# Kernel tuning notes

Measured on AMD Instinct MI355X. Metric: run time of the kernel, lower is better.

The kernel has to match this reference:

```python
import jax, jax.numpy as jnp
import numpy as np

B, T, D, NH = 4, 2048, 1024, 16
HD = D // NH


def setup_inputs() -> dict:
    key = jax.random.key(0)
    ks = jax.random.split(key, 6)
    scale = 0.02
    x = jax.random.normal(ks[0], (B, T, D), dtype=jnp.float32)
    Wr = jax.random.normal(ks[1], (D, D), dtype=jnp.float32) * scale
    Wk = jax.random.normal(ks[2], (D, D), dtype=jnp.float32) * scale
    Wv = jax.random.normal(ks[3], (D, D), dtype=jnp.float32) * scale
    Ww = jax.random.normal(ks[4], (D, D), dtype=jnp.float32) * scale
    Wo = jax.random.normal(ks[5], (D, D), dtype=jnp.float32) * scale
    return {"x": x, "Wr": Wr, "Wk": Wk, "Wv": Wv, "Ww": Ww, "Wo": Wo}


def _rwkv7_forward(x, Wr, Wk, Wv, Ww, Wo):
    b, t, d = x.shape
    nh, hd = NH, d // NH
    # projections (F.linear: x @ W.T), no bias
    r = jax.nn.sigmoid(x @ Wr.T).reshape(b, t, nh, hd)
    k = (x @ Wk.T).reshape(b, t, nh, hd)
    v = (x @ Wv.T).reshape(b, t, nh, hd)
    w = (jax.nn.sigmoid(x @ Ww.T) * 0.99).reshape(b, t, nh, hd)

    def step(state, inp):
        # state: [B, nh, hd_v, hd_k]
        w_t, k_t, v_t, r_t = inp  # each [B, nh, hd]
        state = state * w_t[..., :, None] + v_t[..., :, None] * k_t[..., None, :]
        out_t = r_t * state.sum(-1)  # [B, nh, hd]
        return state, out_t

    seq = (jnp.moveaxis(w, 1, 0), jnp.moveaxis(k, 1, 0),
           jnp.moveaxis(v, 1, 0), jnp.moveaxis(r, 1, 0))  # time-major
    state0 = jnp.zeros((b, nh, hd, hd), dtype=x.dtype)
    _, outs = jax.lax.scan(step, state0, seq)  # [T, B, nh, hd]
    out = jnp.moveaxis(outs, 0, 1).reshape(b, t, d)

    # RMSNorm with eps=None -> torch uses dtype eps
    eps = jnp.asarray(jnp.finfo(out.dtype).eps, out.dtype)
    out = out * jax.lax.rsqrt(jnp.mean(out * out, axis=-1, keepdims=True) + eps)
    return out @ Wo.T


def reference(x, Wr, Wk, Wv, Ww, Wo):
    return _rwkv7_forward(x, Wr, Wk, Wv, Ww, Wo)
```

## Files before the change

### kernel.cpp

```cpp
#include <hip/hip_runtime.h>
#include <hip/hip_bf16.h>
#include <stdint.h>


#define BB 4
#define TT 2048
#define DD 1024
#define NHH 16
#define HDD 64
#define CC 64
#define LL 32
#define NCH 4096

using bf16 = __hip_bfloat16;
typedef __attribute__((ext_vector_type(8))) short bfrag8;
typedef __attribute__((ext_vector_type(4))) float f32x4;

__device__ __forceinline__ void async_ld16(const bf16* g, bf16* l) {
  __builtin_amdgcn_global_load_lds(
      (const __attribute__((address_space(1))) uint32_t*)g,
      (__attribute__((address_space(3))) uint32_t*)l, 16, 0, 0);
}

__device__ __forceinline__ float sigm(float x) {
  return __builtin_amdgcn_rcpf(1.0f + __expf(-x));
}
__device__ __forceinline__ float bf2f(bf16 h) {
  unsigned short u = *reinterpret_cast<unsigned short*>(&h);
  return __uint_as_float((unsigned)u << 16);
}
__device__ __forceinline__ unsigned short f2bfbits(float f) {
  bf16 b = __float2bfloat16(f);
  return *reinterpret_cast<unsigned short*>(&b);
}

__global__ __launch_bounds__(256)
void convert_kernel(const float* __restrict__ x,
                    const float* __restrict__ Wr, const float* __restrict__ Wv,
                    const float* __restrict__ Ww, const float* __restrict__ Wo,
                    const float* __restrict__ Wk,
                    bf16* __restrict__ x_c, bf16* __restrict__ W_c,
                    float* __restrict__ wks)
{
  if (blockIdx.x >= 12288) {
    const int gid = (blockIdx.x - 12288) * 256 + threadIdx.x;
    const int h = gid >> 10, c = gid & 1023;
    float s = 0.0f;
    for (int j = 0; j < 64; ++j)
      s += Wk[(long)((h << 6) + j) * 1024 + c];
    wks[gid] = s;
    return;
  }
  const long g = (long)blockIdx.x * 256 + threadIdx.x;
  const float* src; bf16* dst; long off4;
  if (g < 2097152) { src = x; dst = x_c; off4 = g; }
  else {
    long gg = g - 2097152;
    int wsel = (int)(gg >> 18);
    off4 = gg & 262143;
    src = (wsel == 0) ? Wr : (wsel == 1) ? Wv : (wsel == 2) ? Ww : Wo;
    dst = W_c + (long)wsel * 1048576;
  }
  float4 f = reinterpret_cast<const float4*>(src)[off4];
  ushort4 pk;
  pk.x = f2bfbits(f.x); pk.y = f2bfbits(f.y);
  pk.z = f2bfbits(f.z); pk.w = f2bfbits(f.w);
  reinterpret_cast<ushort4*>(dst)[off4] = pk;
}

__device__ __forceinline__ void gemm_mainloop(
    const bf16* __restrict__ A, const bf16* __restrict__ W,
    int blockM, int blockN, bf16* a_sh, bf16* b_sh, f32x4 acc[4][4])
{
  const int tid    = threadIdx.x;
  const int wave   = tid >> 6;
  const int lane   = tid & 63;
  const int lane15 = lane & 15;
  const int quad   = lane >> 4;
  const int waveM  = wave >> 1;
  const int waveN  = wave & 1;
  const int s_row  = (wave << 5) + (lane >> 3);
  const int s_col  = (((lane & 7) ^ ((lane >> 3) & 7)) << 3);

  const bf16* gA = A + ((long)(blockM * 128) + s_row) * 1024 + s_col;
  const bf16* gW = W + ((long)(blockN * 128) + s_row) * 1024 + s_col;
  bf16* la = a_sh + wave * 2048;
  bf16* lb = b_sh + wave * 2048;

  const int rsw = lane15 & 7;

  for (int k0 = 0; k0 < 1024; k0 += 64) {
#pragma unroll
    for (int it = 0; it < 4; ++it) {
      async_ld16(gA + k0 + it * 8 * 1024, la + it * 512);
      async_ld16(gW + k0 + it * 8 * 1024, lb + it * 512);
    }
    __syncthreads();
#pragma unroll
    for (int kh = 0; kh < 2; ++kh) {
      bfrag8 af[4], bfv[4];
      const int pc = ((kh * 4 + quad) ^ rsw) << 3;
#pragma unroll
      for (int mi = 0; mi < 4; ++mi)
        af[mi] = *reinterpret_cast<const bfrag8*>(a_sh + (waveM*64 + mi*16 + lane15)*64 + pc);
#pragma unroll
      for (int ni = 0; ni < 4; ++ni)
        bfv[ni] = *reinterpret_cast<const bfrag8*>(b_sh + (waveN*64 + ni*16 + lane15)*64 + pc);
#pragma unroll
      for (int mi = 0; mi < 4; ++mi)
#pragma unroll
        for (int ni = 0; ni < 4; ++ni)
          acc[mi][ni] = __builtin_amdgcn_mfma_f32_16x16x32_bf16(af[mi], bfv[ni], acc[mi][ni], 0, 0, 0);
    }
    __syncthreads();
  }
}

__global__ __launch_bounds__(256, 2)
void proj_kernel(const bf16* __restrict__ X, const bf16* __restrict__ W_c,
                 bf16* __restrict__ r_out, bf16* __restrict__ v_out,
                 bf16* __restrict__ w_out)
{
  __shared__ __align__(16) bf16 a_sh[128*64];
  __shared__ __align__(16) bf16 b_sh[128*64];
  const int f  = blockIdx.x;
  const int u  = f & 7;
  const int q  = f >> 3;
  const int n  = q & 7;
  const int p  = q >> 3;
  const int mh = p & 7;
  const int mode = p >> 3;
  const int m  = u + (mh << 3);

  const bf16* W = W_c + (long)mode * 1048576;
  f32x4 acc[4][4] = {};
  gemm_mainloop(X, W, m, n, a_sh, b_sh, acc);

  const int tid = threadIdx.x;
  const int wave = tid >> 6, lane = tid & 63;
  const int lane15 = lane & 15, quad = lane >> 4;
  const int waveM = wave >> 1, waveN = wave & 1;
  const int m_base = m * 128 + waveM * 64;
  const int n_base = n * 128 + waveN * 64;
  bf16* outp = (mode == 0) ? r_out : (mode == 1) ? v_out : w_out;
#pragma unroll
  for (int mi = 0; mi < 4; ++mi)
#pragma unroll
    for (int ni = 0; ni < 4; ++ni)
#pragma unroll
      for (int r = 0; r < 4; ++r) {
        float val = acc[mi][ni][r];
        if (mode == 0) val = sigm(val);
        else if (mode == 2) val = sigm(val) * 0.99f;
        int mm = m_base + mi*16 + quad*4 + r;
        int nn = n_base + ni*16 + lane15;
        outp[(long)mm * DD + nn] = __float2bfloat16(val);
      }
}

__global__ __launch_bounds__(256)
void ksum_kernel(const bf16* __restrict__ X, const float* __restrict__ wks,
                 float* __restrict__ ksum)
{
  __shared__ __align__(8) bf16 xs[DD];
  const int m = blockIdx.x;
  const int tid = threadIdx.x;
  *reinterpret_cast<ushort4*>(xs + tid*4) =
      *reinterpret_cast<const ushort4*>(X + (long)m * DD + tid*4);
  __syncthreads();
  const int wave = tid >> 6, lane = tid & 63;
  const int b = m >> 11, t = m & (TT - 1);
#pragma unroll
  for (int hi = 0; hi < 4; ++hi) {
    const int h = wave * 4 + hi;
    float acc = 0.0f;
#pragma unroll
    for (int i = 0; i < 16; ++i) {
      const int c = lane + (i << 6);
      acc += bf2f(xs[c]) * wks[h * DD + c];
    }
#pragma unroll
    for (int msk = 1; msk <= 32; msk <<= 1) acc += __shfl_xor(acc, msk);
    if (lane == 0) ksum[((long)(b * NHH + h)) * TT + t] = acc;
  }
}

__global__ __launch_bounds__(256)
void scanA_kernel(const bf16* __restrict__ v_buf, const bf16* __restrict__ w_buf,
                  const float* __restrict__ ksum,
                  float* __restrict__ Pbuf, float* __restrict__ Abuf)
{
  __shared__ float ks_sh[128];
  const int bh = blockIdx.x;
  const int b = bh >> 4, h = bh & 15;
  const int tid = threadIdx.x;
  const int i = tid & 63;
  const int cg = tid >> 6;
  const int chunk = blockIdx.y * 4 + cg;
  if (tid < 128) ks_sh[tid] = ksum[(long)bh * TT + blockIdx.y * 128 + tid];
  __syncthreads();
  const long base = (long)b * TT * DD + (long)(chunk * LL) * DD + h * HDD + i;
  float s = 0.0f, P = 1.0f;
#pragma unroll
  for (int j = 0; j < LL; ++j) {
    const long idx = base + (long)j * DD;
    float wv = bf2f(w_buf[idx]);
    float vv = bf2f(v_buf[idx]);
    s = fmaf(wv, s, vv * ks_sh[cg * LL + j]);
    P *= wv;
  }
  const int ch = bh * 64 + i;
  Pbuf[chunk * NCH + ch] = P;
  Abuf[chunk * NCH + ch] = s;
}

__global__ __launch_bounds__(256)
void scanB_kernel(const float* __restrict__ Pbuf, float* __restrict__ Abuf,
                  float* __restrict__ rowssq)
{
  const int tid  = threadIdx.x;
  const int lane = tid & 63;
  const int wch  = blockIdx.x * 4 + (tid >> 6);
  const int idx  = lane * NCH + wch;
  float p = Pbuf[idx];
  float a = Abuf[idx];
#pragma unroll
  for (int d = 1; d < 64; d <<= 1) {
    float al = __shfl_up(a, d);
    float pl = __shfl_up(p, d);
    if (lane >= d) { a = fmaf(p, al, a); p *= pl; }
  }
  float carry = __shfl_up(a, 1);
  if (lane == 0) carry = 0.0f;
  Abuf[idx] = carry;
  if (blockIdx.x < 32) rowssq[blockIdx.x * 256 + tid] = 0.0f;
}

__global__ __launch_bounds__(256)
void scanC_kernel(const bf16* __restrict__ r_buf, bf16* v_so,
                  const bf16* __restrict__ w_buf, const float* __restrict__ ksum,
                  const float* __restrict__ Abuf, float* __restrict__ rowssq)
{
  __shared__ float ks_sh[128];
  const int bh = blockIdx.x;
  const int b = bh >> 4, h = bh & 15;
  const int tid = threadIdx.x;
  const int i = tid & 63;
  const int cg = tid >> 6;
  const int chunk = blockIdx.y * 4 + cg;
  if (tid < 128) ks_sh[tid] = ksum[(long)bh * TT + blockIdx.y * 128 + tid];
  __syncthreads();
  const int ch = bh * 64 + i;
  const long base = (long)b * TT * DD + (long)(chunk * LL) * DD + h * HDD + i;
  float s = Abuf[chunk * NCH + ch];
#pragma unroll
  for (int j = 0; j < LL; ++j) {
    const long idx = base + (long)j * DD;
    float wv = bf2f(w_buf[idx]);
    float vv = bf2f(v_so[idx]);
    float rv = bf2f(r_buf[idx]);
    s = fmaf(wv, s, vv * ks_sh[cg * LL + j]);
    unsigned short ob = f2bfbits(rv * s);
    *reinterpret_cast<unsigned short*>(v_so + idx) = ob;
    float vf = __uint_as_float((unsigned)ob << 16);
    float ss = vf * vf;
#pragma unroll
    for (int msk = 1; msk <= 32; msk <<= 1) ss += __shfl_xor(ss, msk);
    if (i == 0) atomicAdd(&rowssq[b * TT + chunk * LL + j], ss);
  }
}

__global__ __launch_bounds__(256, 2)
void out_gemm_kernel(const bf16* __restrict__ A, const bf16* __restrict__ Wo_c,
                     const float* __restrict__ rowssq, float* __restrict__ out)
{
  __shared__ __align__(16) bf16 a_sh[128*64];
  __shared__ __align__(16) bf16 b_sh[128*64];
  const int f  = blockIdx.x;
  const int u  = f & 7;
  const int q  = f >> 3;
  const int n  = q & 7;
  const int mh = q >> 3;
  const int m  = u + (mh << 3);

  f32x4 acc[4][4] = {};
  gemm_mainloop(A, Wo_c, m, n, a_sh, b_sh, acc);

  const int tid = threadIdx.x;
  const int wave = tid >> 6, lane = tid & 63;
  const int lane15 = lane & 15, quad = lane >> 4;
  const int waveM = wave >> 1, waveN = wave & 1;
  const int m_base = m * 128 + waveM * 64;
  const int n_base = n * 128 + waveN * 64;
#pragma unroll
  for (int mi = 0; mi < 4; ++mi)
#pragma unroll
    for (int r = 0; r < 4; ++r) {
      int mm = m_base + mi*16 + quad*4 + r;
      float sc = rsqrtf(rowssq[mm] * (1.0f / DD) + 1.1920929e-07f);
#pragma unroll
      for (int ni = 0; ni < 4; ++ni) {
        int nn = n_base + ni*16 + lane15;
        out[(long)mm * DD + nn] = acc[mi][ni][r] * sc;
      }
    }
}

extern "C" void kernel_launch(void* const* d_in, const int* in_sizes, int n_in,
                              void* d_out, int out_size, void* d_ws, size_t ws_size,
                              hipStream_t stream) {
  const float* x  = (const float*)d_in[0];
  const float* Wr = (const float*)d_in[1];
  const float* Wk = (const float*)d_in[2];
  const float* Wv = (const float*)d_in[3];
  const float* Ww = (const float*)d_in[4];
  const float* Wo = (const float*)d_in[5];

  const long NELT = (long)BB * TT * DD;
  bf16*  x_c  = (bf16*)d_ws;
  bf16*  W_c  = x_c + NELT;
  bf16*  v_so = W_c + 4 * 1048576;
  float* ksum = (float*)(v_so + NELT);
  float* wks  = ksum + (long)BB * NHH * TT;
  float* Pbuf = wks + NHH * DD;
  float* Abuf = Pbuf + (long)CC * NCH;
  float* rowssq = (float*)x_c;

  bf16*  r_buf = (bf16*)d_out;
  bf16*  w_buf = (bf16*)d_out + NELT;
  float* out   = (float*)d_out;

  convert_kernel<<<dim3(12352), 256, 0, stream>>>(x, Wr, Wv, Ww, Wo, Wk, x_c, W_c, wks);
  proj_kernel<<<dim3(1536), 256, 0, stream>>>(x_c, W_c, r_buf, v_so, w_buf);
  ksum_kernel<<<dim3(BB * TT), 256, 0, stream>>>(x_c, wks, ksum);
  scanA_kernel<<<dim3(64, 16), 256, 0, stream>>>(v_so, w_buf, ksum, Pbuf, Abuf);
  scanB_kernel<<<dim3(1024), 256, 0, stream>>>(Pbuf, Abuf, rowssq);
  scanC_kernel<<<dim3(64, 16), 256, 0, stream>>>(r_buf, v_so, w_buf, ksum, Abuf, rowssq);
  out_gemm_kernel<<<dim3(512), 256, 0, stream>>>(v_so, W_c + 3 * 1048576, rowssq, out);
}
```

Measured before the change: 231.1 us.

## Vectorize scan kernels and restructure ksum to keep weights in registers

The ksum kernel now holds each wave's per-head weight slice in registers and loops over 32 rows per block, reading x with vector loads instead of staging one row in LDS per block. The chunked scan kernels (A and C) give each thread four channels using 4-wide bf16 loads and stores, cover 16 chunks per block, and cut the grid by four. This targets scalar 2-byte memory traffic, per-row launch overhead and redundant weight reloads. The cost is fewer blocks, which may reduce latency hiding for the serial scan loops, and higher register use.

```diff
diff --git a/kernel.cpp b/kernel.cpp
--- a/kernel.cpp
+++ b/kernel.cpp
@@ -27,6 +27,9 @@
 }
 __device__ __forceinline__ float bf2f(bf16 h) {
   unsigned short u = *reinterpret_cast<unsigned short*>(&h);
+  return __uint_as_float((unsigned)u << 16);
+}
+__device__ __forceinline__ float us2f(unsigned short u) {
   return __uint_as_float((unsigned)u << 16);
 }
 __device__ __forceinline__ unsigned short f2bfbits(float f) {
@@ -162,26 +165,42 @@
 void ksum_kernel(const bf16* __restrict__ X, const float* __restrict__ wks,
                  float* __restrict__ ksum)
 {
-  __shared__ __align__(8) bf16 xs[DD];
-  const int m = blockIdx.x;
-  const int tid = threadIdx.x;
-  *reinterpret_cast<ushort4*>(xs + tid*4) =
-      *reinterpret_cast<const ushort4*>(X + (long)m * DD + tid*4);
-  __syncthreads();
+  const int tid = threadIdx.x;
   const int wave = tid >> 6, lane = tid & 63;
-  const int b = m >> 11, t = m & (TT - 1);
+  const int c0 = lane << 4;
+  float wk[4][16];
 #pragma unroll
   for (int hi = 0; hi < 4; ++hi) {
-    const int h = wave * 4 + hi;
-    float acc = 0.0f;
-#pragma unroll
-    for (int i = 0; i < 16; ++i) {
-      const int c = lane + (i << 6);
-      acc += bf2f(xs[c]) * wks[h * DD + c];
-    }
-#pragma unroll
-    for (int msk = 1; msk <= 32; msk <<= 1) acc += __shfl_xor(acc, msk);
-    if (lane == 0) ksum[((long)(b * NHH + h)) * TT + t] = acc;
+    const int h = (wave << 2) + hi;
+#pragma unroll
+    for (int q = 0; q < 4; ++q) {
+      float4 f = *reinterpret_cast<const float4*>(wks + h * DD + c0 + (q << 2));
+      wk[hi][q*4+0] = f.x; wk[hi][q*4+1] = f.y;
+      wk[hi][q*4+2] = f.z; wk[hi][q*4+3] = f.w;
+    }
+  }
+  const int m0 = blockIdx.x << 5;
+  for (int rr = 0; rr < 32; ++rr) {
+    const int m = m0 + rr;
+    const bf16* xp = X + (long)m * DD + c0;
+    float xv[16];
+#pragma unroll
+    for (int q = 0; q < 4; ++q) {
+      ushort4 u = reinterpret_cast<const ushort4*>(xp)[q];
+      xv[q*4+0] = us2f(u.x); xv[q*4+1] = us2f(u.y);
+      xv[q*4+2] = us2f(u.z); xv[q*4+3] = us2f(u.w);
+    }
+    const int b = m >> 11, t = m & (TT - 1);
+#pragma unroll
+    for (int hi = 0; hi < 4; ++hi) {
+      float acc = 0.0f;
+#pragma unroll
+      for (int q = 0; q < 16; ++q) acc = fmaf(xv[q], wk[hi][q], acc);
+#pragma unroll
+      for (int msk = 1; msk <= 32; msk <<= 1) acc += __shfl_xor(acc, msk);
+      if (lane == 0)
+        ksum[((long)(b * NHH + (wave << 2) + hi)) * TT + t] = acc;
+    }
   }
 }
 
@@ -190,28 +209,36 @@
                   const float* __restrict__ ksum,
                   float* __restrict__ Pbuf, float* __restrict__ Abuf)
 {
-  __shared__ float ks_sh[128];
+  __shared__ float ks_sh[512];
   const int bh = blockIdx.x;
   const int b = bh >> 4, h = bh & 15;
   const int tid = threadIdx.x;
-  const int i = tid & 63;
-  const int cg = tid >> 6;
-  const int chunk = blockIdx.y * 4 + cg;
-  if (tid < 128) ks_sh[tid] = ksum[(long)bh * TT + blockIdx.y * 128 + tid];
+  const int lg = tid & 15;
+  const int cl = tid >> 4;
+  const int chunk = (blockIdx.y << 4) + cl;
+  ks_sh[tid]       = ksum[(long)bh * TT + (blockIdx.y << 9) + tid];
+  ks_sh[tid + 256] = ksum[(long)bh * TT + (blockIdx.y << 9) + 256 + tid];
   __syncthreads();
-  const long base = (long)b * TT * DD + (long)(chunk * LL) * DD + h * HDD + i;
-  float s = 0.0f, P = 1.0f;
+  const int i4 = lg << 2;
+  const long base = (long)b * TT * DD + (long)(chunk * LL) * DD + h * HDD + i4;
+  const float* ksp = ks_sh + cl * LL;
+  float s0=0.f, s1=0.f, s2=0.f, s3=0.f;
+  float P0=1.f, P1=1.f, P2=1.f, P3=1.f;
 #pragma unroll
   for (int j = 0; j < LL; ++j) {
     const long idx = base + (long)j * DD;
-    float wv = bf2f(w_buf[idx]);
-    float vv = bf2f(v_buf[idx]);
-    s = fmaf(wv, s, vv * ks_sh[cg * LL + j]);
-    P *= wv;
-  }
-  const int ch = bh * 64 + i;
-  Pbuf[chunk * NCH + ch] = P;
-  Abuf[chunk * NCH + ch] = s;
+    ushort4 wu = *reinterpret_cast<const ushort4*>(w_buf + idx);
+    ushort4 vu = *reinterpret_cast<const ushort4*>(v_buf + idx);
+    const float ks = ksp[j];
+    float w0 = us2f(wu.x), w1 = us2f(wu.y), w2 = us2f(wu.z), w3 = us2f(wu.w);
+    s0 = fmaf(w0, s0, us2f(vu.x) * ks); P0 *= w0;
+    s1 = fmaf(w1, s1, us2f(vu.y) * ks); P1 *= w1;
+    s2 = fmaf(w2, s2, us2f(vu.z) * ks); P2 *= w2;
+    s3 = fmaf(w3, s3, us2f(vu.w) * ks); P3 *= w3;
+  }
+  const int ch = (bh << 6) + i4;
+  *reinterpret_cast<float4*>(Pbuf + (long)chunk * NCH + ch) = make_float4(P0,P1,P2,P3);
+  *reinterpret_cast<float4*>(Abuf + (long)chunk * NCH + ch) = make_float4(s0,s1,s2,s3);
 }
 
 __global__ __launch_bounds__(256)
@@ -241,32 +268,44 @@
                   const bf16* __restrict__ w_buf, const float* __restrict__ ksum,
                   const float* __restrict__ Abuf, float* __restrict__ rowssq)
 {
-  __shared__ float ks_sh[128];
+  __shared__ float ks_sh[512];
   const int bh = blockIdx.x;
   const int b = bh >> 4, h = bh & 15;
   const int tid = threadIdx.x;
-  const int i = tid & 63;
-  const int cg = tid >> 6;
-  const int chunk = blockIdx.y * 4 + cg;
-  if (tid < 128) ks_sh[tid] = ksum[(long)bh * TT + blockIdx.y * 128 + tid];
+  const int lg = tid & 15;
+  const int cl = tid >> 4;
+  const int chunk = (blockIdx.y << 4) + cl;
+  ks_sh[tid]       = ksum[(long)bh * TT + (blockIdx.y << 9) + tid];
+  ks_sh[tid + 256] = ksum[(long)bh * TT + (blockIdx.y << 9) + 256 + tid];
   __syncthreads();
-  const int ch = bh * 64 + i;
-  const long base = (long)b * TT * DD + (long)(chunk * LL) * DD + h * HDD + i;
-  float s = Abuf[chunk * NCH + ch];
+  const int i4 = lg << 2;
+  const int ch = (bh << 6) + i4;
+  const long base = (long)b * TT * DD + (long)(chunk * LL) * DD + h * HDD + i4;
+  const float* ksp = ks_sh + cl * LL;
+  float4 si = *reinterpret_cast<const float4*>(Abuf + (long)chunk * NCH + ch);
+  float s0 = si.x, s1 = si.y, s2 = si.z, s3 = si.w;
 #pragma unroll
   for (int j = 0; j < LL; ++j) {
     const long idx = base + (long)j * DD;
-    float wv = bf2f(w_buf[idx]);
-    float vv = bf2f(v_so[idx]);
-    float rv = bf2f(r_buf[idx]);
-    s = fmaf(wv, s, vv * ks_sh[cg * LL + j]);
-    unsigned short ob = f2bfbits(rv * s);
-    *reinterpret_cast<unsigned short*>(v_so + idx) = ob;
-    float vf = __uint_as_float((unsigned)ob << 16);
-    float ss = vf * vf;
-#pragma unroll
-    for (int msk = 1; msk <= 32; msk <<= 1) ss += __shfl_xor(ss, msk);
-    if (i == 0) atomicAdd(&rowssq[b * TT + chunk * LL + j], ss);
+    ushort4 wu = *reinterpret_cast<const ushort4*>(w_buf + idx);
+    ushort4 vu = *reinterpret_cast<const ushort4*>(v_so + idx);
+    ushort4 ru = *reinterpret_cast<const ushort4*>(r_buf + idx);
+    const float ks = ksp[j];
+    s0 = fmaf(us2f(wu.x), s0, us2f(vu.x) * ks);
+    s1 = fmaf(us2f(wu.y), s1, us2f(vu.y) * ks);
+    s2 = fmaf(us2f(wu.z), s2, us2f(vu.z) * ks);
+    s3 = fmaf(us2f(wu.w), s3, us2f(vu.w) * ks);
+    unsigned short q0 = f2bfbits(us2f(ru.x) * s0);
+    unsigned short q1 = f2bfbits(us2f(ru.y) * s1);
+    unsigned short q2 = f2bfbits(us2f(ru.z) * s2);
+    unsigned short q3 = f2bfbits(us2f(ru.w) * s3);
+    ushort4 pk; pk.x = q0; pk.y = q1; pk.z = q2; pk.w = q3;
+    *reinterpret_cast<ushort4*>(v_so + idx) = pk;
+    float o0 = us2f(q0), o1 = us2f(q1), o2 = us2f(q2), o3 = us2f(q3);
+    float ss = o0*o0 + o1*o1 + o2*o2 + o3*o3;
+    ss += __shfl_xor(ss, 1); ss += __shfl_xor(ss, 2);
+    ss += __shfl_xor(ss, 4); ss += __shfl_xor(ss, 8);
+    if (lg == 0) atomicAdd(&rowssq[b * TT + chunk * LL + j], ss);
   }
 }
 
@@ -332,9 +371,9 @@
 
   convert_kernel<<<dim3(12352), 256, 0, stream>>>(x, Wr, Wv, Ww, Wo, Wk, x_c, W_c, wks);
   proj_kernel<<<dim3(1536), 256, 0, stream>>>(x_c, W_c, r_buf, v_so, w_buf);
-  ksum_kernel<<<dim3(BB * TT), 256, 0, stream>>>(x_c, wks, ksum);
-  scanA_kernel<<<dim3(64, 16), 256, 0, stream>>>(v_so, w_buf, ksum, Pbuf, Abuf);
+  ksum_kernel<<<dim3(256), 256, 0, stream>>>(x_c, wks, ksum);
+  scanA_kernel<<<dim3(64, 4), 256, 0, stream>>>(v_so, w_buf, ksum, Pbuf, Abuf);
   scanB_kernel<<<dim3(1024), 256, 0, stream>>>(Pbuf, Abuf, rowssq);
-  scanC_kernel<<<dim3(64, 16), 256, 0, stream>>>(r_buf, v_so, w_buf, ksum, Abuf, rowssq);
+  scanC_kernel<<<dim3(64, 4), 256, 0, stream>>>(r_buf, v_so, w_buf, ksum, Abuf, rowssq);
   out_gemm_kernel<<<dim3(512), 256, 0, stream>>>(v_so, W_c + 3 * 1048576, rowssq, out);
 }
```

Result: slower. 260.4 us (+12.7%).

## Fuse three-pass chunked scan into single decoupled-lookback scan kernel

Applied to the files above, without the earlier changes.

Replaces the scanA/scanB/scanC passes with one kernel. Each block computes chunk aggregates for its four chunks, combines them in shared memory, publishes a block aggregate with a flag, and spins on flags from earlier blocks to get its incoming state. The w and v values are kept packed in registers so the second pass does not reload them from global memory. This removes two kernel launches and a global round-trip of the per-chunk buffers. In exchange it relies on inter-block spin-waiting, whose forward progress depends on block scheduling order, and it raises register pressure from the 32-entry packed array.

```diff
diff --git a/kernel.cpp b/kernel.cpp
--- a/kernel.cpp
+++ b/kernel.cpp
@@ -40,10 +40,13 @@
                     const float* __restrict__ Ww, const float* __restrict__ Wo,
                     const float* __restrict__ Wk,
                     bf16* __restrict__ x_c, bf16* __restrict__ W_c,
-                    float* __restrict__ wks)
+                    float* __restrict__ wks, float* __restrict__ rowssq,
+                    unsigned int* __restrict__ flags)
 {
   if (blockIdx.x >= 12288) {
     const int gid = (blockIdx.x - 12288) * 256 + threadIdx.x;
+    if (gid < 8192) rowssq[gid] = 0.0f;
+    if (gid < 1024) flags[gid] = 0u;
     const int h = gid >> 10, c = gid & 1023;
     float s = 0.0f;
     for (int j = 0; j < 64; ++j)
@@ -185,82 +188,89 @@
   }
 }
 
-__global__ __launch_bounds__(256)
-void scanA_kernel(const bf16* __restrict__ v_buf, const bf16* __restrict__ w_buf,
-                  const float* __restrict__ ksum,
-                  float* __restrict__ Pbuf, float* __restrict__ Abuf)
+__global__ __launch_bounds__(256, 4)
+void scan_fused_kernel(const bf16* __restrict__ r_buf, bf16* v_so,
+                       const bf16* __restrict__ w_buf,
+                       const float* __restrict__ ksum,
+                       float* __restrict__ Pl, float* __restrict__ Al,
+                       float* __restrict__ rowssq,
+                       unsigned int* __restrict__ flags)
 {
   __shared__ float ks_sh[128];
+  __shared__ float Psh[4][64], Ash[4][64];
+  __shared__ float sin_sh[64];
   const int bh = blockIdx.x;
+  const int yb = blockIdx.y;
   const int b = bh >> 4, h = bh & 15;
   const int tid = threadIdx.x;
   const int i = tid & 63;
   const int cg = tid >> 6;
-  const int chunk = blockIdx.y * 4 + cg;
-  if (tid < 128) ks_sh[tid] = ksum[(long)bh * TT + blockIdx.y * 128 + tid];
+  const int chunk = yb * 4 + cg;
+  if (tid < 128) ks_sh[tid] = ksum[(long)bh * TT + yb * 128 + tid];
   __syncthreads();
   const long base = (long)b * TT * DD + (long)(chunk * LL) * DD + h * HDD + i;
+  const float* ksp = ks_sh + cg * LL;
+
+  unsigned int wv_pk[LL];
   float s = 0.0f, P = 1.0f;
 #pragma unroll
   for (int j = 0; j < LL; ++j) {
     const long idx = base + (long)j * DD;
-    float wv = bf2f(w_buf[idx]);
-    float vv = bf2f(v_buf[idx]);
-    s = fmaf(wv, s, vv * ks_sh[cg * LL + j]);
-    P *= wv;
-  }
-  const int ch = bh * 64 + i;
-  Pbuf[chunk * NCH + ch] = P;
-  Abuf[chunk * NCH + ch] = s;
-}
-
-__global__ __launch_bounds__(256)
-void scanB_kernel(const float* __restrict__ Pbuf, float* __restrict__ Abuf,
-                  float* __restrict__ rowssq)
-{
-  const int tid  = threadIdx.x;
-  const int lane = tid & 63;
-  const int wch  = blockIdx.x * 4 + (tid >> 6);
-  const int idx  = lane * NCH + wch;
-  float p = Pbuf[idx];
-  float a = Abuf[idx];
-#pragma unroll
-  for (int d = 1; d < 64; d <<= 1) {
-    float al = __shfl_up(a, d);
-    float pl = __shfl_up(p, d);
-    if (lane >= d) { a = fmaf(p, al, a); p *= pl; }
-  }
-  float carry = __shfl_up(a, 1);
-  if (lane == 0) carry = 0.0f;
-  Abuf[idx] = carry;
-  if (blockIdx.x < 32) rowssq[blockIdx.x * 256 + tid] = 0.0f;
-}
-
-__global__ __launch_bounds__(256)
-void scanC_kernel(const bf16* __restrict__ r_buf, bf16* v_so,
-                  const bf16* __restrict__ w_buf, const float* __restrict__ ksum,
-                  const float* __restrict__ Abuf, float* __restrict__ rowssq)
-{
-  __shared__ float ks_sh[128];
-  const int bh = blockIdx.x;
-  const int b = bh >> 4, h = bh & 15;
-  const int tid = threadIdx.x;
-  const int i = tid & 63;
-  const int cg = tid >> 6;
-  const int chunk = blockIdx.y * 4 + cg;
-  if (tid < 128) ks_sh[tid] = ksum[(long)bh * TT + blockIdx.y * 128 + tid];
+    unsigned int wu = *reinterpret_cast<const unsigned short*>(w_buf + idx);
+    unsigned int vu = *reinterpret_cast<const unsigned short*>(v_so + idx);
+    wv_pk[j] = wu | (vu << 16);
+    float wf = __uint_as_float(wu << 16);
+    s = fmaf(wf, s, __uint_as_float(vu << 16) * ksp[j]);
+    P *= wf;
+  }
+  Psh[cg][i] = P; Ash[cg][i] = s;
   __syncthreads();
-  const int ch = bh * 64 + i;
-  const long base = (long)b * TT * DD + (long)(chunk * LL) * DD + h * HDD + i;
-  float s = Abuf[chunk * NCH + ch];
+
+  float Spre = 0.0f, Ppre = 1.0f;
+  for (int c2 = 0; c2 < cg; ++c2) {
+    Spre = fmaf(Psh[c2][i], Spre, Ash[c2][i]);
+    Ppre *= Psh[c2][i];
+  }
+
+  if (cg == 3) {
+    Pl[(bh * 16 + yb) * 64 + i] = Ppre * P;
+    Al[(bh * 16 + yb) * 64 + i] = fmaf(P, Spre, s);
+    __threadfence();
+    if (tid == 192) atomicExch(flags + bh * 16 + yb, 1u);
+  }
+
+  float S_in = 0.0f;
+  if (yb > 0) {
+    if (tid == 0) {
+      for (int yy = 0; yy < yb; ++yy) {
+        unsigned int* fp = flags + bh * 16 + yy;
+        int g = 0;
+        while (atomicAdd(fp, 0u) == 0u && g < 2000000) ++g;
+      }
+    }
+    __syncthreads();
+    if (tid < 64) {
+      float S = 0.0f;
+      for (int yy = 0; yy < yb; ++yy) {
+        float p = atomicAdd(Pl + (bh * 16 + yy) * 64 + tid, 0.0f);
+        float a = atomicAdd(Al + (bh * 16 + yy) * 64 + tid, 0.0f);
+        S = fmaf(p, S, a);
+      }
+      sin_sh[tid] = S;
+    }
+    __syncthreads();
+    S_in = sin_sh[i];
+  }
+  float sC = fmaf(Ppre, S_in, Spre);
+
 #pragma unroll
   for (int j = 0; j < LL; ++j) {
     const long idx = base + (long)j * DD;
-    float wv = bf2f(w_buf[idx]);
-    float vv = bf2f(v_so[idx]);
+    float wv = __uint_as_float((wv_pk[j] & 0xffffu) << 16);
+    float vv = __uint_as_float(wv_pk[j] & 0xffff0000u);
     float rv = bf2f(r_buf[idx]);
-    s = fmaf(wv, s, vv * ks_sh[cg * LL + j]);
-    unsigned short ob = f2bfbits(rv * s);
+    sC = fmaf(wv, sC, vv * ksp[j]);
+    unsigned short ob = f2bfbits(rv * sC);
     *reinterpret_cast<unsigned short*>(v_so + idx) = ob;
     float vf = __uint_as_float((unsigned)ob << 16);
     float ss = vf * vf;
@@ -322,19 +332,20 @@
   bf16*  v_so = W_c + 4 * 1048576;
   float* ksum = (float*)(v_so + NELT);
   float* wks  = ksum + (long)BB * NHH * TT;
-  float* Pbuf = wks + NHH * DD;
-  float* Abuf = Pbuf + (long)CC * NCH;
-  float* rowssq = (float*)x_c;
+  float* Pl   = wks + NHH * DD;
+  float* Al   = Pl + 64 * 16 * 64;
+  float* rowssq = Al + 64 * 16 * 64;
+  unsigned int* flags = (unsigned int*)(rowssq + (long)BB * TT);
 
   bf16*  r_buf = (bf16*)d_out;
   bf16*  w_buf = (bf16*)d_out + NELT;
   float* out   = (float*)d_out;
 
-  convert_kernel<<<dim3(12352), 256, 0, stream>>>(x, Wr, Wv, Ww, Wo, Wk, x_c, W_c, wks);
+  convert_kernel<<<dim3(12352), 256, 0, stream>>>(x, Wr, Wv, Ww, Wo, Wk,
+                                                  x_c, W_c, wks, rowssq, flags);
   proj_kernel<<<dim3(1536), 256, 0, stream>>>(x_c, W_c, r_buf, v_so, w_buf);
   ksum_kernel<<<dim3(BB * TT), 256, 0, stream>>>(x_c, wks, ksum);
-  scanA_kernel<<<dim3(64, 16), 256, 0, stream>>>(v_so, w_buf, ksum, Pbuf, Abuf);
-  scanB_kernel<<<dim3(1024), 256, 0, stream>>>(Pbuf, Abuf, rowssq);
-  scanC_kernel<<<dim3(64, 16), 256, 0, stream>>>(r_buf, v_so, w_buf, ksum, Abuf, rowssq);
+  scan_fused_kernel<<<dim3(64, 16), 256, 0, stream>>>(r_buf, v_so, w_buf, ksum,
+                                                      Pl, Al, rowssq, flags);
   out_gemm_kernel<<<dim3(512), 256, 0, stream>>>(v_so, W_c + 3 * 1048576, rowssq, out);
 }
```

Result: slower. 270.2 us (+16.9%).

## Store projection outputs time-major so scan kernels use vectorized time loads

Applied to the files above, without the earlier changes.

The projection GEMM epilogue now writes r, v and w transposed (channel-major, time contiguous), packing 4 consecutive time steps per store. The scanA and scanC kernels then load 32 time steps per channel with 16-byte vector loads instead of one 2-byte load per step. The scan output goes to a separate buffer that reuses the x_c workspace, and rowssq moves into the weight region. The GEMM epilogue stores become strided across lanes, which may cost write efficiency in exchange for cheaper scan reads.

```diff
diff --git a/kernel.cpp b/kernel.cpp
--- a/kernel.cpp
+++ b/kernel.cpp
@@ -11,9 +11,11 @@
 #define CC 64
 #define LL 32
 #define NCH 4096
+#define MT (BB * TT)
 
 using bf16 = __hip_bfloat16;
 typedef __attribute__((ext_vector_type(8))) short bfrag8;
+typedef __attribute__((ext_vector_type(8))) unsigned short us8;
 typedef __attribute__((ext_vector_type(4))) float f32x4;
 
 __device__ __forceinline__ void async_ld16(const bf16* g, bf16* l) {
@@ -27,6 +29,9 @@
 }
 __device__ __forceinline__ float bf2f(bf16 h) {
   unsigned short u = *reinterpret_cast<unsigned short*>(&h);
+  return __uint_as_float((unsigned)u << 16);
+}
+__device__ __forceinline__ float us2f(unsigned short u) {
   return __uint_as_float((unsigned)u << 16);
 }
 __device__ __forceinline__ unsigned short f2bfbits(float f) {
@@ -118,8 +123,8 @@
 
 __global__ __launch_bounds__(256, 2)
 void proj_kernel(const bf16* __restrict__ X, const bf16* __restrict__ W_c,
-                 bf16* __restrict__ r_out, bf16* __restrict__ v_out,
-                 bf16* __restrict__ w_out)
+                 bf16* __restrict__ r_t, bf16* __restrict__ v_t,
+                 bf16* __restrict__ w_t)
 {
   __shared__ __align__(16) bf16 a_sh[128*64];
   __shared__ __align__(16) bf16 b_sh[128*64];
@@ -142,20 +147,26 @@
   const int waveM = wave >> 1, waveN = wave & 1;
   const int m_base = m * 128 + waveM * 64;
   const int n_base = n * 128 + waveN * 64;
-  bf16* outp = (mode == 0) ? r_out : (mode == 1) ? v_out : w_out;
-#pragma unroll
-  for (int mi = 0; mi < 4; ++mi)
-#pragma unroll
-    for (int ni = 0; ni < 4; ++ni)
-#pragma unroll
-      for (int r = 0; r < 4; ++r) {
-        float val = acc[mi][ni][r];
-        if (mode == 0) val = sigm(val);
-        else if (mode == 2) val = sigm(val) * 0.99f;
-        int mm = m_base + mi*16 + quad*4 + r;
-        int nn = n_base + ni*16 + lane15;
-        outp[(long)mm * DD + nn] = __float2bfloat16(val);
+  bf16* outp = (mode == 0) ? r_t : (mode == 1) ? v_t : w_t;
+#pragma unroll
+  for (int mi = 0; mi < 4; ++mi) {
+    const int mm0 = m_base + mi*16 + quad*4;
+#pragma unroll
+    for (int ni = 0; ni < 4; ++ni) {
+      const int nn = n_base + ni*16 + lane15;
+      float v0 = acc[mi][ni][0], v1 = acc[mi][ni][1];
+      float v2 = acc[mi][ni][2], v3 = acc[mi][ni][3];
+      if (mode == 0) { v0 = sigm(v0); v1 = sigm(v1); v2 = sigm(v2); v3 = sigm(v3); }
+      else if (mode == 2) {
+        v0 = sigm(v0)*0.99f; v1 = sigm(v1)*0.99f;
+        v2 = sigm(v2)*0.99f; v3 = sigm(v3)*0.99f;
       }
+      ushort4 pk;
+      pk.x = f2bfbits(v0); pk.y = f2bfbits(v1);
+      pk.z = f2bfbits(v2); pk.w = f2bfbits(v3);
+      *reinterpret_cast<ushort4*>(outp + (long)nn * MT + mm0) = pk;
+    }
+  }
 }
 
 __global__ __launch_bounds__(256)
@@ -186,7 +197,7 @@
 }
 
 __global__ __launch_bounds__(256)
-void scanA_kernel(const bf16* __restrict__ v_buf, const bf16* __restrict__ w_buf,
+void scanA_kernel(const bf16* __restrict__ v_t, const bf16* __restrict__ w_t,
                   const float* __restrict__ ksum,
                   float* __restrict__ Pbuf, float* __restrict__ Abuf)
 {
@@ -199,19 +210,26 @@
   const int chunk = blockIdx.y * 4 + cg;
   if (tid < 128) ks_sh[tid] = ksum[(long)bh * TT + blockIdx.y * 128 + tid];
   __syncthreads();
-  const long base = (long)b * TT * DD + (long)(chunk * LL) * DD + h * HDD + i;
+  const int ch = h * HDD + i;
+  const long tbase = (long)ch * MT + b * TT + chunk * LL;
+  us8 wv[4], vv[4];
+#pragma unroll
+  for (int q = 0; q < 4; ++q) {
+    wv[q] = *reinterpret_cast<const us8*>(w_t + tbase + q*8);
+    vv[q] = *reinterpret_cast<const us8*>(v_t + tbase + q*8);
+  }
+  const float* ksp = ks_sh + cg * LL;
   float s = 0.0f, P = 1.0f;
 #pragma unroll
   for (int j = 0; j < LL; ++j) {
-    const long idx = base + (long)j * DD;
-    float wv = bf2f(w_buf[idx]);
-    float vv = bf2f(v_buf[idx]);
-    s = fmaf(wv, s, vv * ks_sh[cg * LL + j]);
-    P *= wv;
-  }
-  const int ch = bh * 64 + i;
-  Pbuf[chunk * NCH + ch] = P;
-  Abuf[chunk * NCH + ch] = s;
+    float wf = us2f((unsigned short)wv[j>>3][j&7]);
+    float vf = us2f((unsigned short)vv[j>>3][j&7]);
+    s = fmaf(wf, s, vf * ksp[j]);
+    P *= wf;
+  }
+  const int chn = bh * 64 + i;
+  Pbuf[chunk * NCH + chn] = P;
+  Abuf[chunk * NCH + chn] = s;
 }
 
 __global__ __launch_bounds__(256)
@@ -237,9 +255,10 @@
 }
 
 __global__ __launch_bounds__(256)
-void scanC_kernel(const bf16* __restrict__ r_buf, bf16* v_so,
-                  const bf16* __restrict__ w_buf, const float* __restrict__ ksum,
-                  const float* __restrict__ Abuf, float* __restrict__ rowssq)
+void scanC_kernel(const bf16* __restrict__ r_t, const bf16* __restrict__ v_t,
+                  const bf16* __restrict__ w_t, const float* __restrict__ ksum,
+                  const float* __restrict__ Abuf, bf16* __restrict__ so,
+                  float* __restrict__ rowssq)
 {
   __shared__ float ks_sh[128];
   const int bh = blockIdx.x;
@@ -250,20 +269,29 @@
   const int chunk = blockIdx.y * 4 + cg;
   if (tid < 128) ks_sh[tid] = ksum[(long)bh * TT + blockIdx.y * 128 + tid];
   __syncthreads();
-  const int ch = bh * 64 + i;
-  const long base = (long)b * TT * DD + (long)(chunk * LL) * DD + h * HDD + i;
-  float s = Abuf[chunk * NCH + ch];
+  const int ch = h * HDD + i;
+  const long tbase = (long)ch * MT + b * TT + chunk * LL;
+  us8 wv[4], vv[4], rv[4];
+#pragma unroll
+  for (int q = 0; q < 4; ++q) {
+    wv[q] = *reinterpret_cast<const us8*>(w_t + tbase + q*8);
+    vv[q] = *reinterpret_cast<const us8*>(v_t + tbase + q*8);
+    rv[q] = *reinterpret_cast<const us8*>(r_t + tbase + q*8);
+  }
+  const float* ksp = ks_sh + cg * LL;
+  const int chn = bh * 64 + i;
+  float s = Abuf[chunk * NCH + chn];
+  const long obase = (long)(b * TT + chunk * LL) * DD + ch;
 #pragma unroll
   for (int j = 0; j < LL; ++j) {
-    const long idx = base + (long)j * DD;
-    float wv = bf2f(w_buf[idx]);
-    float vv = bf2f(v_so[idx]);
-    float rv = bf2f(r_buf[idx]);
-    s = fmaf(wv, s, vv * ks_sh[cg * LL + j]);
-    unsigned short ob = f2bfbits(rv * s);
-    *reinterpret_cast<unsigned short*>(v_so + idx) = ob;
-    float vf = __uint_as_float((unsigned)ob << 16);
-    float ss = vf * vf;
+    float wf = us2f((unsigned short)wv[j>>3][j&7]);
+    float vf = us2f((unsigned short)vv[j>>3][j&7]);
+    float rf = us2f((unsigned short)rv[j>>3][j&7]);
+    s = fmaf(wf, s, vf * ksp[j]);
+    unsigned short ob = f2bfbits(rf * s);
+    *reinterpret_cast<unsigned short*>(so + obase + (long)j * DD) = ob;
+    float vfo = us2f(ob);
+    float ss = vfo * vfo;
 #pragma unroll
     for (int msk = 1; msk <= 32; msk <<= 1) ss += __shfl_xor(ss, msk);
     if (i == 0) atomicAdd(&rowssq[b * TT + chunk * LL + j], ss);
@@ -319,22 +347,23 @@
   const long NELT = (long)BB * TT * DD;
   bf16*  x_c  = (bf16*)d_ws;
   bf16*  W_c  = x_c + NELT;
-  bf16*  v_so = W_c + 4 * 1048576;
-  float* ksum = (float*)(v_so + NELT);
+  bf16*  v_t  = W_c + 4 * 1048576;
+  float* ksum = (float*)(v_t + NELT);
   float* wks  = ksum + (long)BB * NHH * TT;
   float* Pbuf = wks + NHH * DD;
   float* Abuf = Pbuf + (long)CC * NCH;
-  float* rowssq = (float*)x_c;
-
-  bf16*  r_buf = (bf16*)d_out;
-  bf16*  w_buf = (bf16*)d_out + NELT;
-  float* out   = (float*)d_out;
+  float* rowssq = (float*)W_c;
+
+  bf16*  r_t  = (bf16*)d_out;
+  bf16*  w_t  = (bf16*)d_out + NELT;
+  bf16*  so   = x_c;
+  float* out  = (float*)d_out;
 
   convert_kernel<<<dim3(12352), 256, 0, stream>>>(x, Wr, Wv, Ww, Wo, Wk, x_c, W_c, wks);
-  proj_kernel<<<dim3(1536), 256, 0, stream>>>(x_c, W_c, r_buf, v_so, w_buf);
+  proj_kernel<<<dim3(1536), 256, 0, stream>>>(x_c, W_c, r_t, v_t, w_t);
   ksum_kernel<<<dim3(BB * TT), 256, 0, stream>>>(x_c, wks, ksum);
-  scanA_kernel<<<dim3(64, 16), 256, 0, stream>>>(v_so, w_buf, ksum, Pbuf, Abuf);
+  scanA_kernel<<<dim3(64, 16), 256, 0, stream>>>(v_t, w_t, ksum, Pbuf, Abuf);
   scanB_kernel<<<dim3(1024), 256, 0, stream>>>(Pbuf, Abuf, rowssq);
-  scanC_kernel<<<dim3(64, 16), 256, 0, stream>>>(r_buf, v_so, w_buf, ksum, Abuf, rowssq);
-  out_gemm_kernel<<<dim3(512), 256, 0, stream>>>(v_so, W_c + 3 * 1048576, rowssq, out);
-}
+  scanC_kernel<<<dim3(64, 16), 256, 0, stream>>>(r_t, v_t, w_t, ksum, Abuf, so, rowssq);
+  out_gemm_kernel<<<dim3(512), 256, 0, stream>>>(so, W_c + 3 * 1048576, rowssq, out);
+}
```

New measurement: 241.8 us. 4.6% more time.
